# Optimization experiments

Measured on AMD Instinct MI355X. Metric: run time of the kernel, lower is better.

## Reference

```python
import jax, jax.numpy as jnp
import numpy as np

B, S, D = 8, 4096, 256
L, H = 4, 8
HD = D // H  # head_dim = 32
EPS = 1e-5


def layer_norm(x, gamma, beta):
    mu = jnp.mean(x, axis=-1, keepdims=True)
    var = jnp.mean(jnp.square(x - mu), axis=-1, keepdims=True)
    return (x - mu) * jax.lax.rsqrt(var + EPS) * gamma + beta


def setup_inputs() -> dict:
    key = jax.random.key(0)
    ks = jax.random.split(key, 9)
    sc = 0.02
    x = jax.random.normal(ks[0], (B, S, D), dtype=jnp.float32)
    # per-head projection weights, torch Linear convention: (out=head_dim, in=D)
    Wq = jax.random.normal(ks[1], (L, H, HD, D), dtype=jnp.float32) * sc
    Wk = jax.random.normal(ks[2], (L, H, HD, D), dtype=jnp.float32) * sc
    Wv = jax.random.normal(ks[3], (L, H, HD, D), dtype=jnp.float32) * sc
    W1 = jax.random.normal(ks[4], (L, D, D), dtype=jnp.float32) * sc
    b1 = jax.random.normal(ks[5], (L, D), dtype=jnp.float32) * sc
    W2 = jax.random.normal(ks[6], (L, D, D), dtype=jnp.float32) * sc
    b2 = jax.random.normal(ks[7], (L, D), dtype=jnp.float32) * sc
    gamma = jnp.ones((D,), dtype=jnp.float32)
    beta = jnp.zeros((D,), dtype=jnp.float32)
    return {"processed_grid_repr": x, "Wq": Wq, "Wk": Wk, "Wv": Wv,
            "W1": W1, "b1": b1, "W2": W2, "b2": b2,
            "gamma": gamma, "beta": beta}


def reference(processed_grid_repr, Wq, Wk, Wv, W1, b1, W2, b2, gamma, beta):
    out = processed_grid_repr  # (B, S, D)
    scale = 1.0 / jnp.sqrt(jnp.float32(S))  # original scales by sqrt(seq_len)
    for l in range(L):
        h = layer_norm(out, gamma, beta)
        # all heads at once: (B, H, S, HD)
        Q = jnp.einsum('bsd,hed->bhse', h, Wq[l])
        K = jnp.einsum('bsd,hed->bhse', h, Wk[l])
        V = jnp.einsum('bsd,hed->bhse', h, Wv[l])
        # original does key.reshape(B, HD, S) (a RESHAPE, not a transpose)
        Kr = K.reshape(B, H, HD, S)
        # original einsum 'bqq,bqd->bqd' only uses the diagonal of QK^r,
        # so compute only the diagonal: diag[b,h,q] = sum_e Q[b,h,q,e]*Kr[b,h,e,q]
        diag = jnp.einsum('bhse,bhes->bhs', Q, Kr) * scale
        attn = diag[..., None] * V  # (B, H, S, HD)
        # concat heads along last dim (head order preserved)
        msa_out = attn.transpose(0, 2, 1, 3).reshape(B, S, D)
        attended = msa_out + out
        m = layer_norm(attended, gamma, beta)
        m = jax.nn.gelu(m @ W1[l].T + b1[l], approximate=False)
        m = jax.nn.gelu(m @ W2[l].T + b2[l], approximate=False)
        out = m + attended
    # final: layer norm of CLS-like token 0
    return layer_norm(out[:, 0, :], gamma, beta)  # (B, D)
```

## Files before the change

### kernel.cpp

```cpp
#include <hip/hip_runtime.h>
#include <hip/hip_bf16.h>
#include <hip/hip_fp16.h>

typedef _Float16 half_t;
typedef _Float16 half8 __attribute__((ext_vector_type(8)));
typedef _Float16 half4 __attribute__((ext_vector_type(4)));
typedef float f32x4 __attribute__((ext_vector_type(4)));

#define BB 8
#define SS 4096
#define DD 256
#define HH 8
#define LL 4
#define MTOT (BB*SS)

__device__ inline float gelu_f(float v) { return 0.5f * v * (1.0f + erff(v * 0.70710678118f)); }
__device__ inline half8 splat8(half_t v) { return (half8){v, v, v, v, v, v, v, v}; }

__device__ __forceinline__ void gload16(const half_t* g, half_t* l) {
    __builtin_amdgcn_global_load_lds(
        (const __attribute__((address_space(1))) void*)g,
        (__attribute__((address_space(3))) void*)l, 16, 0, 0);
}

__global__ __launch_bounds__(256) void prep_weights(
    const float* __restrict__ Wq, const float* __restrict__ Wk, const float* __restrict__ Wv,
    const float* __restrict__ W1, const float* __restrict__ b1,
    const float* __restrict__ W2, const float* __restrict__ b2,
    const float* __restrict__ gamma, const float* __restrict__ beta,
    half_t* __restrict__ Wall, half_t* __restrict__ W1h, half_t* __restrict__ W2h,
    float* __restrict__ bqkv, float* __restrict__ b1f, float* __restrict__ b2f)
{
    int blk = blockIdx.x;
    int l = blk / 5, type = blk % 5;
    int o = threadIdx.x;
    const float* src = (type == 0 ? Wq : type == 1 ? Wk : type == 2 ? Wv : type == 3 ? W1 : W2)
                       + ((size_t)l * 256 + o) * 256;
    half_t* dsth = (type < 3) ? Wall + ((size_t)(l * 3 + type) * 256 + o) * 256
                 : (type == 3) ? W1h + ((size_t)l * 256 + o) * 256
                               : W2h + ((size_t)l * 256 + o) * 256;
    float acc = 0.f;
    for (int d4 = 0; d4 < 64; ++d4) {
        float4 w = *(const float4*)(src + d4 * 4);
        half4 hv;
        if (type == 4) {
            hv = half4{ (half_t)w.x, (half_t)w.y, (half_t)w.z, (half_t)w.w };
        } else {
            float4 g = *(const float4*)(gamma + d4 * 4);
            float4 bt = *(const float4*)(beta + d4 * 4);
            acc += w.x * bt.x + w.y * bt.y + w.z * bt.z + w.w * bt.w;
            hv = half4{ (half_t)(w.x * g.x), (half_t)(w.y * g.y), (half_t)(w.z * g.z), (half_t)(w.w * g.w) };
        }
        *(half4*)(dsth + d4 * 4) = hv;
    }
    if (type < 3) bqkv[(l * 3 + type) * 256 + o] = acc;
    else if (type == 3) b1f[l * 256 + o] = b1[l * 256 + o] + acc;
    else b2f[l * 256 + o] = b2[l * 256 + o];
}

__global__ __launch_bounds__(256) void cvt_x_stats(const float* __restrict__ in,
                                                   half_t* __restrict__ out,
                                                   float2* __restrict__ st0,
                                                   float2* __restrict__ st1) {
    int wave = threadIdx.x >> 6, lane = threadIdx.x & 63;
    int row = blockIdx.x * 4 + wave;
    const float* ip = in + (size_t)row * DD + lane * 4;
    float4 v = *(const float4*)ip;
    half4 h = { (half_t)v.x, (half_t)v.y, (half_t)v.z, (half_t)v.w };
    *(half4*)(out + (size_t)row * DD + lane * 4) = h;
    float s1 = v.x + v.y + v.z + v.w;
    float s2 = v.x * v.x + v.y * v.y + v.z * v.z + v.w * v.w;
    #pragma unroll
    for (int m = 32; m; m >>= 1) {
        s1 += __shfl_xor(s1, m);
        s2 += __shfl_xor(s2, m);
    }
    if (lane == 0) {
        st0[row] = make_float2(s1, s2);
        st1[row] = make_float2(0.f, 0.f);
    }
}

__device__ inline void xcd_remap(int& bx, int& by, int& bz) {
    int lin = blockIdx.x + gridDim.x * (blockIdx.y + gridDim.y * blockIdx.z);
    int nyz = gridDim.y * gridDim.z;
    int xcd = lin & 7;
    int slot = lin >> 3;
    int yz = slot % nyz;
    int xi = slot / nyz;
    bx = xcd + 8 * xi;
    by = yz % gridDim.y;
    bz = yz / gridDim.y;
}

template<int NORM, int EPI, int STATS>
__global__ __launch_bounds__(256) void gemm128(const half_t* __restrict__ A,
                                               const float2* __restrict__ st0,
                                               const float2* __restrict__ st1,
                                               const half_t* __restrict__ Wbase,
                                               const float* __restrict__ biasBase,
                                               const half_t* __restrict__ resid,
                                               half_t* __restrict__ o0,
                                               half_t* __restrict__ o1,
                                               half_t* __restrict__ o2,
                                               float2* __restrict__ outSt0,
                                               float2* __restrict__ outSt1) {
    const int t = threadIdx.x, lane = t & 63, wavei = t >> 6;
    const int wm = wavei >> 1, wn = wavei & 1, r = lane & 15, g = lane >> 4;
    int bx, by, bz;
    xcd_remap(bx, by, bz);
    const int row0 = bx * 128, col0 = by * 128;
    const half_t* W = Wbase + (size_t)bz * 65536;
    const float* bias = biasBase + bz * 256;
    half_t* outp = (bz == 0) ? o0 : ((bz == 1) ? o1 : o2);

    __shared__ __align__(16) half_t lds[16384];

    const half_t* Ag = A + (size_t)row0 * DD;
    const half_t* Wg = W + (size_t)col0 * DD;

    half8 sA[4], bA[4];
    if (NORM) {
        #pragma unroll
        for (int mt = 0; mt < 4; ++mt) {
            int row = row0 + wm * 64 + mt * 16 + r;
            float2 p0 = st0[row], p1 = st1[row];
            float s1 = p0.x + p1.x, s2 = p0.y + p1.y;
            float mu = s1 * (1.0f / DD);
            float var = s2 * (1.0f / DD) - mu * mu;
            float rs = rsqrtf(var + 1e-5f);
            sA[mt] = splat8((half_t)rs);
            bA[mt] = splat8((half_t)(-mu * rs));
        }
    }

    int rowS[4], chS[4];
    #pragma unroll
    for (int i = 0; i < 4; ++i) {
        int G = i * 256 + t;
        rowS[i] = G >> 3;
        chS[i] = ((G & 7) ^ (rowS[i] & 7)) * 8;
    }

    f32x4 acc[4][4];
    #pragma unroll
    for (int i = 0; i < 4; ++i)
        #pragma unroll
        for (int j = 0; j < 4; ++j) acc[i][j] = (f32x4){0.f, 0.f, 0.f, 0.f};

    #pragma unroll
    for (int stp = 0; stp < 4; ++stp) {
        int kk = stp * 64;
        #pragma unroll
        for (int i = 0; i < 4; ++i) {
            int G = i * 256 + t;
            gload16(Ag + (size_t)rowS[i] * DD + kk + chS[i], &lds[G * 8]);
            gload16(Wg + (size_t)rowS[i] * DD + kk + chS[i], &lds[8192 + G * 8]);
        }
        __syncthreads();
        #pragma unroll
        for (int ks = 0; ks < 2; ++ks) {
            half8 af[4], bf[4];
            #pragma unroll
            for (int mt = 0; mt < 4; ++mt) {
                int rw = wm * 64 + mt * 16 + r;
                int cc = (ks * 4 + g) ^ (rw & 7);
                half8 raw = *(const half8*)&lds[rw * 64 + cc * 8];
                af[mt] = NORM ? (half8)(raw * sA[mt] + bA[mt]) : raw;
            }
            #pragma unroll
            for (int nt = 0; nt < 4; ++nt) {
                int rw = wn * 64 + nt * 16 + r;
                int cc = (ks * 4 + g) ^ (rw & 7);
                bf[nt] = *(const half8*)&lds[8192 + rw * 64 + cc * 8];
            }
            #pragma unroll
            for (int mt = 0; mt < 4; ++mt)
                #pragma unroll
                for (int nt = 0; nt < 4; ++nt)
                    acc[mt][nt] = __builtin_amdgcn_mfma_f32_16x16x32_f16(af[mt], bf[nt], acc[mt][nt], 0, 0, 0);
        }
        __syncthreads();
    }

    half_t* ldsT = &lds[0];
    #pragma unroll
    for (int mt = 0; mt < 4; ++mt) {
        #pragma unroll
        for (int nt = 0; nt < 4; ++nt) {
            int colL = wn * 64 + nt * 16 + r;
            float bv = bias[col0 + colL];
            #pragma unroll
            for (int j = 0; j < 4; ++j) {
                int rowL = wm * 64 + mt * 16 + g * 4 + j;
                float v = acc[mt][nt][j] + bv;
                if (EPI != 0) v = gelu_f(v);
                ldsT[rowL * 128 + (colL ^ ((rowL & 12) << 2))] = (half_t)v;
            }
        }
    }
    __syncthreads();
    const int l15 = lane & 15, lg = lane >> 4;
    float2* outSt = (by == 0) ? outSt0 : outSt1;
    #pragma unroll
    for (int i = 0; i < 8; ++i) {
        int rowL = wavei * 32 + lg * 8 + i;
        int colL = l15 * 8;
        half8 v = *(const half8*)&ldsT[rowL * 128 + (colL ^ ((rowL & 12) << 2))];
        size_t off = (size_t)(row0 + rowL) * DD + col0 + colL;
        if (EPI == 2) {
            half8 rsd = *(const half8*)&resid[off];
            #pragma unroll
            for (int q = 0; q < 8; ++q) v[q] = (half_t)((float)v[q] + (float)rsd[q]);
        }
        *(half8*)&outp[off] = v;
        if (STATS) {
            float s1 = 0.f, s2 = 0.f;
            #pragma unroll
            for (int q = 0; q < 8; ++q) { float f = (float)v[q]; s1 += f; s2 += f * f; }
            #pragma unroll
            for (int m = 1; m <= 8; m <<= 1) {
                s1 += __shfl_xor(s1, m);
                s2 += __shfl_xor(s2, m);
            }
            if (l15 == 0) outSt[row0 + rowL] = make_float2(s1, s2);
        }
    }
}

__global__ __launch_bounds__(256) void diag_tiled(const half_t* __restrict__ Q,
                                                  const half_t* __restrict__ K,
                                                  float* __restrict__ dg) {
    int blk = blockIdx.x;
    int sblk = blk & 15, h = (blk >> 4) & 7, b = blk >> 7;
    int t = threadIdx.x;
    __shared__ __align__(16) half_t kt[256 * 32];
    int r0b = sblk * 8;
    {
        int e = t >> 3, del = t & 7;
        const half_t* kp = K + ((size_t)b * SS + e * 128 + r0b + del) * DD + h * 32;
        int4* dst = (int4*)&kt[t * 32];
        const int4* sp = (const int4*)kp;
        dst[0] = sp[0]; dst[1] = sp[1]; dst[2] = sp[2]; dst[3] = sp[3];
    }
    __syncthreads();
    int s = sblk * 256 + t;
    const half8* q8 = (const half8*)(Q + ((size_t)b * SS + s) * DD + h * 32);
    int cs = t & 31, ds = t >> 5;
    float sum = 0.f;
    #pragma unroll
    for (int v = 0; v < 4; ++v) {
        half8 qq = q8[v];
        #pragma unroll
        for (int j = 0; j < 8; ++j) {
            int e = v * 8 + j;
            sum += (float)qq[j] * (float)kt[(e * 8 + ds) * 32 + cs];
        }
    }
    dg[((size_t)b << 15) | ((size_t)h << 12) | s] = sum * 0.015625f;
}

__global__ __launch_bounds__(256) void attn_stat(const half_t* __restrict__ resid,
                                                 const half_t* __restrict__ V,
                                                 const float* __restrict__ dg,
                                                 half_t* __restrict__ att,
                                                 float2* __restrict__ st0,
                                                 float2* __restrict__ st1) {
    int wave = threadIdx.x >> 6, lane = threadIdx.x & 63;
    int row = blockIdx.x * 4 + wave;
    int b = row >> 12, s = row & (SS - 1);
    int h = lane >> 3;
    float dgv = dg[((size_t)b << 15) | ((size_t)h << 12) | s];
    size_t base = (size_t)row * DD + lane * 4;
    half4 rs4 = *(const half4*)(resid + base);
    half4 v4 = *(const half4*)(V + base);
    float a0 = (float)rs4[0] + dgv * (float)v4[0];
    float a1 = (float)rs4[1] + dgv * (float)v4[1];
    float a2 = (float)rs4[2] + dgv * (float)v4[2];
    float a3 = (float)rs4[3] + dgv * (float)v4[3];
    half4 at = { (half_t)a0, (half_t)a1, (half_t)a2, (half_t)a3 };
    *(half4*)(att + base) = at;
    float s1 = a0 + a1 + a2 + a3;
    float s2 = a0 * a0 + a1 * a1 + a2 * a2 + a3 * a3;
    #pragma unroll
    for (int m = 32; m; m >>= 1) {
        s1 += __shfl_xor(s1, m);
        s2 += __shfl_xor(s2, m);
    }
    if (lane == 0) {
        st0[row] = make_float2(s1, s2);
        st1[row] = make_float2(0.f, 0.f);
    }
}

__global__ __launch_bounds__(256) void final_ln_kernel(const half_t* __restrict__ cur,
                                                       float* __restrict__ out,
                                                       const float* __restrict__ gamma,
                                                       const float* __restrict__ beta) {
    int b = blockIdx.x;
    int d = threadIdx.x;
    float x = (float)cur[(size_t)b * SS * DD + d];
    float s1 = x, s2 = x * x;
    #pragma unroll
    for (int m = 32; m; m >>= 1) {
        s1 += __shfl_xor(s1, m);
        s2 += __shfl_xor(s2, m);
    }
    __shared__ float ls1[4], ls2[4];
    int wave = threadIdx.x >> 6, lane = threadIdx.x & 63;
    if (lane == 0) { ls1[wave] = s1; ls2[wave] = s2; }
    __syncthreads();
    float t1 = ls1[0] + ls1[1] + ls1[2] + ls1[3];
    float t2 = ls2[0] + ls2[1] + ls2[2] + ls2[3];
    float mu = t1 * (1.0f / DD);
    float var = t2 * (1.0f / DD) - mu * mu;
    float rs = rsqrtf(var + 1e-5f);
    out[(size_t)b * DD + d] = (x - mu) * rs * gamma[d] + beta[d];
}

extern "C" void kernel_launch(void* const* d_in, const int* in_sizes, int n_in,
                              void* d_out, int out_size, void* d_ws, size_t ws_size,
                              hipStream_t stream) {
    const float* x     = (const float*)d_in[0];
    const float* Wq    = (const float*)d_in[1];
    const float* Wk    = (const float*)d_in[2];
    const float* Wv    = (const float*)d_in[3];
    const float* W1    = (const float*)d_in[4];
    const float* b1    = (const float*)d_in[5];
    const float* W2    = (const float*)d_in[6];
    const float* b2    = (const float*)d_in[7];
    const float* gamma = (const float*)d_in[8];
    const float* beta  = (const float*)d_in[9];

    char* p = (char*)d_ws;
    half_t* x16  = (half_t*)p; p += (size_t)MTOT * DD * 2;
    half_t* cur  = (half_t*)p; p += (size_t)MTOT * DD * 2;
    half_t* att  = (half_t*)p; p += (size_t)MTOT * DD * 2;
    half_t* Qb   = (half_t*)p; p += (size_t)MTOT * DD * 2;
    half_t* Kb   = (half_t*)p; p += (size_t)MTOT * DD * 2;
    half_t* Vb   = (half_t*)p; p += (size_t)MTOT * DD * 2;
    half_t* m1   = (half_t*)p; p += (size_t)MTOT * DD * 2;
    float*  dgp  = (float*)p;  p += (size_t)BB * HH * SS * 4;
    float2* stA0 = (float2*)p; p += (size_t)MTOT * 8;
    float2* stA1 = (float2*)p; p += (size_t)MTOT * 8;
    float2* stB0 = (float2*)p; p += (size_t)MTOT * 8;
    float2* stB1 = (float2*)p; p += (size_t)MTOT * 8;
    half_t* Wall = (half_t*)p; p += (size_t)LL * 3 * 65536 * 2;
    half_t* W1h  = (half_t*)p; p += (size_t)LL * 65536 * 2;
    half_t* W2h  = (half_t*)p; p += (size_t)LL * 65536 * 2;
    float*  bqkv = (float*)p;  p += (size_t)LL * 3 * 256 * 4;
    float*  b1f  = (float*)p;  p += (size_t)LL * 256 * 4;
    float*  b2f  = (float*)p;  p += (size_t)LL * 256 * 4;

    prep_weights<<<LL * 5, 256, 0, stream>>>(Wq, Wk, Wv, W1, b1, W2, b2, gamma, beta,
                                             Wall, W1h, W2h, bqkv, b1f, b2f);
    cvt_x_stats<<<MTOT / 4, 256, 0, stream>>>(x, x16, stA0, stA1);

    const half_t* curin = x16;
    for (int l = 0; l < LL; ++l) {
        gemm128<1, 0, 0><<<dim3(256, 2, 3), 256, 0, stream>>>(
            curin, stA0, stA1, Wall + (size_t)l * 3 * 65536, bqkv + l * 3 * 256,
            nullptr, Qb, Kb, Vb, nullptr, nullptr);
        diag_tiled<<<1024, 256, 0, stream>>>(Qb, Kb, dgp);
        attn_stat<<<MTOT / 4, 256, 0, stream>>>(curin, Vb, dgp, att, stB0, stB1);
        gemm128<1, 1, 0><<<dim3(256, 2, 1), 256, 0, stream>>>(
            att, stB0, stB1, W1h + (size_t)l * 65536, b1f + l * 256,
            nullptr, m1, m1, m1, nullptr, nullptr);
        gemm128<0, 2, 1><<<dim3(256, 2, 1), 256, 0, stream>>>(
            m1, nullptr, nullptr, W2h + (size_t)l * 65536, b2f + l * 256,
            att, cur, cur, cur, stA0, stA1);
        curin = cur;
    }
    final_ln_kernel<<<BB, 256, 0, stream>>>(cur, (float*)d_out, gamma, beta);
}
```

Baseline: 347.7 us.

## Fuse diagonal attention score with residual attention and row stats kernel

Merges the diag_tiled and attn_stat kernels into one diag_attn kernel per (batch, 64-row chunk). K rows are loaded into LDS with global_load_lds, all 8 head diagonals are computed per row into shared memory, and then the residual plus diag*V output and the LayerNorm sums are produced in the same block. This removes the float diag buffer round trip and one launch per layer. The cost is a 32KB LDS footprint per block and only 512 blocks, which may reduce occupancy.

```diff
diff --git a/kernel.cpp b/kernel.cpp
--- a/kernel.cpp
+++ b/kernel.cpp
@@ -228,68 +228,79 @@
     }
 }
 
-__global__ __launch_bounds__(256) void diag_tiled(const half_t* __restrict__ Q,
-                                                  const half_t* __restrict__ K,
-                                                  float* __restrict__ dg) {
-    int blk = blockIdx.x;
-    int sblk = blk & 15, h = (blk >> 4) & 7, b = blk >> 7;
-    int t = threadIdx.x;
-    __shared__ __align__(16) half_t kt[256 * 32];
-    int r0b = sblk * 8;
-    {
-        int e = t >> 3, del = t & 7;
-        const half_t* kp = K + ((size_t)b * SS + e * 128 + r0b + del) * DD + h * 32;
-        int4* dst = (int4*)&kt[t * 32];
-        const int4* sp = (const int4*)kp;
-        dst[0] = sp[0]; dst[1] = sp[1]; dst[2] = sp[2]; dst[3] = sp[3];
-    }
-    __syncthreads();
-    int s = sblk * 256 + t;
-    const half8* q8 = (const half8*)(Q + ((size_t)b * SS + s) * DD + h * 32);
-    int cs = t & 31, ds = t >> 5;
-    float sum = 0.f;
-    #pragma unroll
-    for (int v = 0; v < 4; ++v) {
-        half8 qq = q8[v];
-        #pragma unroll
-        for (int j = 0; j < 8; ++j) {
-            int e = v * 8 + j;
-            sum += (float)qq[j] * (float)kt[(e * 8 + ds) * 32 + cs];
-        }
-    }
-    dg[((size_t)b << 15) | ((size_t)h << 12) | s] = sum * 0.015625f;
-}
-
-__global__ __launch_bounds__(256) void attn_stat(const half_t* __restrict__ resid,
-                                                 const half_t* __restrict__ V,
-                                                 const float* __restrict__ dg,
+__global__ __launch_bounds__(256) void diag_attn(const half_t* __restrict__ Qb,
+                                                 const half_t* __restrict__ Kb,
+                                                 const half_t* __restrict__ Vb,
+                                                 const half_t* __restrict__ curg,
                                                  half_t* __restrict__ att,
                                                  float2* __restrict__ st0,
                                                  float2* __restrict__ st1) {
-    int wave = threadIdx.x >> 6, lane = threadIdx.x & 63;
-    int row = blockIdx.x * 4 + wave;
-    int b = row >> 12, s = row & (SS - 1);
-    int h = lane >> 3;
-    float dgv = dg[((size_t)b << 15) | ((size_t)h << 12) | s];
-    size_t base = (size_t)row * DD + lane * 4;
-    half4 rs4 = *(const half4*)(resid + base);
-    half4 v4 = *(const half4*)(V + base);
-    float a0 = (float)rs4[0] + dgv * (float)v4[0];
-    float a1 = (float)rs4[1] + dgv * (float)v4[1];
-    float a2 = (float)rs4[2] + dgv * (float)v4[2];
-    float a3 = (float)rs4[3] + dgv * (float)v4[3];
-    half4 at = { (half_t)a0, (half_t)a1, (half_t)a2, (half_t)a3 };
-    *(half4*)(att + base) = at;
-    float s1 = a0 + a1 + a2 + a3;
-    float s2 = a0 * a0 + a1 * a1 + a2 * a2 + a3 * a3;
-    #pragma unroll
-    for (int m = 32; m; m >>= 1) {
-        s1 += __shfl_xor(s1, m);
-        s2 += __shfl_xor(s2, m);
-    }
-    if (lane == 0) {
-        st0[row] = make_float2(s1, s2);
-        st1[row] = make_float2(0.f, 0.f);
+    int blk = blockIdx.x;
+    int sc = blk & 63, b = blk >> 6;
+    int t = threadIdx.x;
+    __shared__ __align__(16) half_t kt[64 * 256];
+    __shared__ float dgl[8][64];
+
+    #pragma unroll
+    for (int i = 0; i < 8; ++i) {
+        int G = i * 256 + t;
+        int rl = G >> 5, cg = G & 31;
+        int e = rl >> 1, q = rl & 1;
+        gload16(Kb + ((size_t)b * SS + e * 128 + sc * 2 + q) * DD + cg * 8, &kt[G * 8]);
+    }
+    __syncthreads();
+
+    {
+        int u = t >> 2, hh = (t & 3) * 2;
+        int s = sc * 64 + u;
+        const half8* qp = (const half8*)(Qb + ((size_t)b * SS + s) * DD + hh * 32);
+        float dv0 = 0.f, dv1 = 0.f;
+        #pragma unroll
+        for (int v = 0; v < 4; ++v) {
+            half8 q0 = qp[v];
+            half8 q1 = qp[4 + v];
+            #pragma unroll
+            for (int j = 0; j < 8; ++j) {
+                int e = v * 8 + j;
+                int rbase = (e * 2 + (u >> 5)) * 256 + (u & 31);
+                dv0 += (float)q0[j] * (float)kt[rbase + hh * 32];
+                dv1 += (float)q1[j] * (float)kt[rbase + (hh + 1) * 32];
+            }
+        }
+        dgl[hh][u] = dv0 * 0.015625f;
+        dgl[hh + 1][u] = dv1 * 0.015625f;
+    }
+    __syncthreads();
+
+    {
+        int u = t >> 2, qq = t & 3;
+        int grow = sc * 64 + u;
+        size_t base = ((size_t)b * SS + grow) * DD + qq * 64;
+        float s1 = 0.f, s2 = 0.f;
+        #pragma unroll
+        for (int i = 0; i < 2; ++i) {
+            float dgv = dgl[qq * 2 + i][u];
+            #pragma unroll
+            for (int v = 0; v < 4; ++v) {
+                half8 c8 = *(const half8*)(curg + base + i * 32 + v * 8);
+                half8 v8 = *(const half8*)(Vb + base + i * 32 + v * 8);
+                half8 a8;
+                #pragma unroll
+                for (int j = 0; j < 8; ++j) {
+                    float a = (float)c8[j] + dgv * (float)v8[j];
+                    s1 += a; s2 += a * a;
+                    a8[j] = (half_t)a;
+                }
+                *(half8*)(att + base + i * 32 + v * 8) = a8;
+            }
+        }
+        s1 += __shfl_xor(s1, 1); s2 += __shfl_xor(s2, 1);
+        s1 += __shfl_xor(s1, 2); s2 += __shfl_xor(s2, 2);
+        if (qq == 0) {
+            int row = b * SS + grow;
+            st0[row] = make_float2(s1, s2);
+            st1[row] = make_float2(0.f, 0.f);
+        }
     }
 }
 
@@ -340,7 +351,6 @@
     half_t* Kb   = (half_t*)p; p += (size_t)MTOT * DD * 2;
     half_t* Vb   = (half_t*)p; p += (size_t)MTOT * DD * 2;
     half_t* m1   = (half_t*)p; p += (size_t)MTOT * DD * 2;
-    float*  dgp  = (float*)p;  p += (size_t)BB * HH * SS * 4;
     float2* stA0 = (float2*)p; p += (size_t)MTOT * 8;
     float2* stA1 = (float2*)p; p += (size_t)MTOT * 8;
     float2* stB0 = (float2*)p; p += (size_t)MTOT * 8;
@@ -361,8 +371,7 @@
         gemm128<1, 0, 0><<<dim3(256, 2, 3), 256, 0, stream>>>(
             curin, stA0, stA1, Wall + (size_t)l * 3 * 65536, bqkv + l * 3 * 256,
             nullptr, Qb, Kb, Vb, nullptr, nullptr);
-        diag_tiled<<<1024, 256, 0, stream>>>(Qb, Kb, dgp);
-        attn_stat<<<MTOT / 4, 256, 0, stream>>>(curin, Vb, dgp, att, stB0, stB1);
+        diag_attn<<<BB * 64, 256, 0, stream>>>(Qb, Kb, Vb, curin, att, stB0, stB1);
         gemm128<1, 1, 0><<<dim3(256, 2, 1), 256, 0, stream>>>(
             att, stB0, stB1, W1h + (size_t)l * 65536, b1f + l * 256,
             nullptr, m1, m1, m1, nullptr, nullptr);
```

After: 361.3 us. 1.04x slower.
